# Kernel optimization log

Hardware: AMD Instinct MI355X
Metric: run time of the kernel (lower is better)

## Reference

```python
import jax, jax.numpy as jnp
import numpy as np

N = 100000   # nodes
E = 1000000  # directed edges (before self-loops)
G = 512      # graphs in the batch
NEG_SLOPE = 0.2
EPS = 1e-5


def setup_inputs() -> dict:
    key = jax.random.key(0)
    ks = jax.random.split(key, 24)
    r = lambda i, shape, s=0.1: (jax.random.normal(ks[i], shape) * s).astype(jnp.float32)
    return {
        'x': jax.random.normal(ks[0], (N, 27), dtype=jnp.float32),
        'edge_index': jax.random.randint(ks[1], (2, E), 0, N, dtype=jnp.int32),
        'batch': jnp.sort(jax.random.randint(ks[2], (N,), 0, G, dtype=jnp.int32)),
        # GATv2Conv(26, 32, heads=2)
        'Wl1': r(3, (26, 64)), 'bl1': jnp.zeros(64, jnp.float32),
        'Wr1': r(4, (26, 64)), 'br1': jnp.zeros(64, jnp.float32),
        'att1': r(5, (2, 32)), 'b1': jnp.zeros(64, jnp.float32),
        'g1': jnp.ones(64, jnp.float32), 'be1': jnp.zeros(64, jnp.float32),
        # GATv2Conv(64, 32, heads=1)
        'Wl2': r(6, (64, 32)), 'bl2': jnp.zeros(32, jnp.float32),
        'Wr2': r(7, (64, 32)), 'br2': jnp.zeros(32, jnp.float32),
        'att2': r(8, (1, 32)), 'b2': jnp.zeros(32, jnp.float32),
        'g2': jnp.ones(32, jnp.float32), 'be2': jnp.zeros(32, jnp.float32),
        # gate_nn: 32 -> 16 -> 1
        'Wg1': r(9, (32, 16)), 'bg1': jnp.zeros(16, jnp.float32),
        'Wg2': r(10, (16, 1)), 'bg2': jnp.zeros(1, jnp.float32),
        # final head: 33 -> 16 -> 1
        'Wh1': r(11, (33, 16)), 'bh1': jnp.zeros(16, jnp.float32),
        'Wh2': r(12, (16, 1)), 'bh2': jnp.zeros(1, jnp.float32),
    }


def _gatv2(x, Wl, bl, Wr, br, att, bias, src, dst, heads, ch):
    n = x.shape[0]
    xl = (x @ Wl + bl).reshape(n, heads, ch)  # source projection (messages)
    xr = (x @ Wr + br).reshape(n, heads, ch)  # target projection
    e = jax.nn.leaky_relu(xl[src] + xr[dst], NEG_SLOPE)      # [Etot, H, C]
    logits = jnp.einsum('ehc,hc->eh', e, att)                 # [Etot, H]
    m = jax.ops.segment_max(logits, dst, num_segments=n)
    a = jnp.exp(logits - m[dst])
    z = jax.ops.segment_sum(a, dst, num_segments=n)
    a = a / (z[dst] + 1e-16)
    out = jax.ops.segment_sum(xl[src] * a[:, :, None], dst, num_segments=n)
    return out.reshape(n, heads * ch) + bias


def _batchnorm(h, gamma, beta):
    mu = h.mean(axis=0)
    var = jnp.var(h, axis=0)  # biased, matches torch normalization
    return (h - mu) * jax.lax.rsqrt(var + EPS) * gamma + beta


def reference(x, edge_index, batch, Wl1, bl1, Wr1, br1, att1, b1, g1, be1,
              Wl2, bl2, Wr2, br2, att2, b2, g2, be2,
              Wg1, bg1, Wg2, bg2, Wh1, bh1, Wh2, bh2):
    n = x.shape[0]
    loops = jnp.arange(n, dtype=edge_index.dtype)
    src = jnp.concatenate([edge_index[0], loops])
    dst = jnp.concatenate([edge_index[1], loops])
    x_no_cost = jnp.concatenate([x[:, :24], x[:, 25:]], axis=1)  # [N, 26]
    h = jax.nn.elu(_batchnorm(_gatv2(x_no_cost, Wl1, bl1, Wr1, br1, att1, b1, src, dst, 2, 32), g1, be1))
    # dropout is identity in eval mode
    h = jax.nn.elu(_batchnorm(_gatv2(h, Wl2, bl2, Wr2, br2, att2, b2, src, dst, 1, 32), g2, be2))
    # attentional aggregation: gate MLP + segment softmax over graphs
    gate = jax.nn.relu(h @ Wg1 + bg1) @ Wg2 + bg2               # [N, 1]
    gm = jax.ops.segment_max(gate, batch, num_segments=G)
    ga = jnp.exp(gate - gm[batch])
    gz = jax.ops.segment_sum(ga, batch, num_segments=G)
    ga = ga / (gz[batch] + 1e-16)
    h_pooled = jax.ops.segment_sum(ga * h, batch, num_segments=G)  # [G, 32]
    counts = jax.ops.segment_sum(jnp.ones((n, 1), x.dtype), batch, num_segments=G)
    root_costs = jax.ops.segment_sum(x[:, 24:25], batch, num_segments=G) / jnp.maximum(counts, 1.0)
    combined = jnp.concatenate([h_pooled, root_costs], axis=1)   # [G, 33]
    return jax.nn.relu(combined @ Wh1 + bh1) @ Wh2 + bh2         # [G, 1]
```

## Files before the change

kernel.cpp:

```cpp
#include <hip/hip_runtime.h>
#include <hip/hip_fp16.h>
#include <math.h>

#define NEG 0.2f
#define BN_EPS 1e-5f
#define BKT_W 256
#define CHUNK 4096


__global__ __launch_bounds__(256, 4)
void hist_proj1_kernel(const int* __restrict__ ei, int E, int nbh, int nbkt,
                       int* __restrict__ cnt,
                       const float* __restrict__ in, int in_stride,
                       const float* __restrict__ Wl, const float* __restrict__ bl,
                       const float* __restrict__ Wr, const float* __restrict__ br,
                       __half* __restrict__ outl, __half* __restrict__ outr, int n)
{
    __shared__ int hist[512];
    __shared__ float xs[32][28];

    if (blockIdx.x < nbh) {
        const int bid = blockIdx.x;
        for (int i = threadIdx.x; i < nbkt; i += 256) hist[i] = 0;
        __syncthreads();
        const int g0 = bid * (CHUNK / 4);
        #pragma unroll
        for (int it = 0; it < CHUNK / 1024; ++it) {
            int e = (g0 + it * 256 + threadIdx.x) * 4;
            if (e + 3 < E) {
                int4 d4 = *(const int4*)(ei + E + e);
                atomicAdd(&hist[d4.x >> 8], 1);
                atomicAdd(&hist[d4.y >> 8], 1);
                atomicAdd(&hist[d4.z >> 8], 1);
                atomicAdd(&hist[d4.w >> 8], 1);
            } else {
                for (int k = 0; k < 4; ++k)
                    if (e + k < E) atomicAdd(&hist[ei[E + e + k] >> 8], 1);
            }
        }
        __syncthreads();
        for (int i = threadIdx.x; i < nbkt; i += 256) cnt[(size_t)i * nbh + bid] = hist[i];
    } else {
        constexpr int K = 26, OC = 64, NCG = 32;
        const int row0 = (blockIdx.x - nbh) * 32;
        for (int i = threadIdx.x; i < 32 * K; i += 256) {
            int r = i / K, k = i - r * K;
            int row = row0 + r;
            float v = 0.f;
            if (row < n) {
                int sc = (k < 24) ? k : k + 1;
                v = in[(size_t)row * in_stride + sc];
            }
            xs[r][k] = v;
        }
        __syncthreads();

        const int cg = threadIdx.x % NCG;
        const int rg = threadIdx.x / NCG;
        const int c4 = cg * 4;
        const bool left = (c4 < OC);
        const float* __restrict__ Wp = left ? Wl : Wr;
        const int cc = left ? c4 : c4 - OC;
        const float4 b4 = *(const float4*)((left ? bl : br) + cc);

        float acc[4][4];
        #pragma unroll
        for (int ri = 0; ri < 4; ++ri) {
            acc[ri][0] = b4.x; acc[ri][1] = b4.y; acc[ri][2] = b4.z; acc[ri][3] = b4.w;
        }
        #pragma unroll 1
        for (int kb = 0; kb < K / 4; ++kb) {
            const float4 w0 = *(const float4*)(Wp + (size_t)(kb * 4 + 0) * OC + cc);
            const float4 w1 = *(const float4*)(Wp + (size_t)(kb * 4 + 1) * OC + cc);
            const float4 w2 = *(const float4*)(Wp + (size_t)(kb * 4 + 2) * OC + cc);
            const float4 w3 = *(const float4*)(Wp + (size_t)(kb * 4 + 3) * OC + cc);
            #pragma unroll
            for (int ri = 0; ri < 4; ++ri) {
                const float4 xv = *(const float4*)(&xs[rg * 4 + ri][kb * 4]);
                acc[ri][0] += xv.x * w0.x + xv.y * w1.x + xv.z * w2.x + xv.w * w3.x;
                acc[ri][1] += xv.x * w0.y + xv.y * w1.y + xv.z * w2.y + xv.w * w3.y;
                acc[ri][2] += xv.x * w0.z + xv.y * w1.z + xv.z * w2.z + xv.w * w3.z;
                acc[ri][3] += xv.x * w0.w + xv.y * w1.w + xv.z * w2.w + xv.w * w3.w;
            }
        }
        #pragma unroll
        for (int k = 24; k < K; ++k) {
            const float4 wk = *(const float4*)(Wp + (size_t)k * OC + cc);
            #pragma unroll
            for (int ri = 0; ri < 4; ++ri) {
                const float xk = xs[rg * 4 + ri][k];
                acc[ri][0] += xk * wk.x; acc[ri][1] += xk * wk.y;
                acc[ri][2] += xk * wk.z; acc[ri][3] += xk * wk.w;
            }
        }
        __half* __restrict__ outp = left ? outl : outr;
        #pragma unroll
        for (int ri = 0; ri < 4; ++ri) {
            const int row = row0 + rg * 4 + ri;
            if (row >= n) continue;
            union { uint2 u; __half2 h[2]; } o;
            o.h[0] = __float22half2_rn(make_float2(acc[ri][0], acc[ri][1]));
            o.h[1] = __float22half2_rn(make_float2(acc[ri][2], acc[ri][3]));
            *(uint2*)(outp + (size_t)row * OC + cc) = o.u;
        }
    }
}

__global__ __launch_bounds__(256)
void scan_block_kernel(const int* __restrict__ in, int* __restrict__ out,
                       int* __restrict__ bsum, int n)
{
    __shared__ int s[256];
    int i = blockIdx.x * 256 + threadIdx.x;
    int v = (i < n) ? in[i] : 0;
    s[threadIdx.x] = v;
    __syncthreads();
    for (int off = 1; off < 256; off <<= 1) {
        int t = (threadIdx.x >= off) ? s[threadIdx.x - off] : 0;
        __syncthreads();
        s[threadIdx.x] += t;
        __syncthreads();
    }
    if (i < n) out[i + 1] = s[threadIdx.x];
    if (threadIdx.x == 255) bsum[blockIdx.x] = s[255];
}

__global__ __launch_bounds__(512)
void scan_sums_kernel(int* __restrict__ bsum, int nb)
{
    __shared__ int s[512];
    int v = (threadIdx.x < nb) ? bsum[threadIdx.x] : 0;
    s[threadIdx.x] = v;
    __syncthreads();
    for (int off = 1; off < 512; off <<= 1) {
        int t = (threadIdx.x >= off) ? s[threadIdx.x - off] : 0;
        __syncthreads();
        s[threadIdx.x] += t;
        __syncthreads();
    }
    if (threadIdx.x < nb) bsum[threadIdx.x] = s[threadIdx.x] - v;
}

__global__ __launch_bounds__(256)
void scan_add_kernel(int* __restrict__ out, const int* __restrict__ bsum, int n)
{
    int i = blockIdx.x * 256 + threadIdx.x;
    if (i < n) out[i + 1] += bsum[blockIdx.x];
    if (i == 0) out[0] = 0;
}

__global__ __launch_bounds__(256)
void scat_kernel(const int* __restrict__ ei, int E, int nbh, int nbkt,
                 const int* __restrict__ base, int2* __restrict__ pairs)
{
    __shared__ int fill[512];
    __shared__ int lbase[512];
    for (int i = threadIdx.x; i < nbkt; i += 256) {
        fill[i]  = 0;
        lbase[i] = base[(size_t)i * nbh + blockIdx.x];
    }
    __syncthreads();
    const int g0 = blockIdx.x * (CHUNK / 4);
    #pragma unroll
    for (int it = 0; it < CHUNK / 1024; ++it) {
        int e = (g0 + it * 256 + threadIdx.x) * 4;
        if (e + 3 < E) {
            int4 s4 = *(const int4*)(ei + e);
            int4 d4 = *(const int4*)(ei + E + e);
            int b, r;
            b = d4.x >> 8; r = atomicAdd(&fill[b], 1); pairs[lbase[b] + r] = make_int2(s4.x, d4.x);
            b = d4.y >> 8; r = atomicAdd(&fill[b], 1); pairs[lbase[b] + r] = make_int2(s4.y, d4.y);
            b = d4.z >> 8; r = atomicAdd(&fill[b], 1); pairs[lbase[b] + r] = make_int2(s4.z, d4.z);
            b = d4.w >> 8; r = atomicAdd(&fill[b], 1); pairs[lbase[b] + r] = make_int2(s4.w, d4.w);
        } else {
            for (int k = 0; k < 4; ++k) {
                if (e + k < E) {
                    int s = ei[e + k], d = ei[E + e + k];
                    int b = d >> 8;
                    int r = atomicAdd(&fill[b], 1);
                    pairs[lbase[b] + r] = make_int2(s, d);
                }
            }
        }
    }
}

__global__ __launch_bounds__(256)
void bucket_build_kernel(const int2* __restrict__ pairs, const int* __restrict__ base,
                         int nbh, int nbkt, int n, int E,
                         int* __restrict__ rowptr, int* __restrict__ srcs,
                         int* __restrict__ perm)
{
    const int b     = blockIdx.x;
    const int start = base[(size_t)b * nbh];
    const int end   = base[(size_t)(b + 1) * nbh];
    __shared__ int hist[256], sc[256], dcnt[64], dbase[64];
    hist[threadIdx.x] = 0;
    if (threadIdx.x < 64) dcnt[threadIdx.x] = 0;
    __syncthreads();
    for (int j = start + threadIdx.x; j < end; j += 256)
        atomicAdd(&hist[pairs[j].y & 255], 1);
    __syncthreads();
    const int v = hist[threadIdx.x];
    sc[threadIdx.x] = v;
    __syncthreads();
    for (int off = 1; off < 256; off <<= 1) {
        int t = (threadIdx.x >= off) ? sc[threadIdx.x - off] : 0;
        __syncthreads();
        sc[threadIdx.x] += t;
        __syncthreads();
    }
    const int excl = sc[threadIdx.x] - v;
    const int d = b * 256 + threadIdx.x;
    int bin = 0, rnk = 0;
    if (d < n) {
        rowptr[d] = start + excl;
        bin = min(v, 63);
        rnk = atomicAdd(&dcnt[bin], 1);
    }
    if (b == nbkt - 1 && threadIdx.x == 0) rowptr[n] = E;
    __syncthreads();
    hist[threadIdx.x] = excl;
    __syncthreads();
    for (int j = start + threadIdx.x; j < end; j += 256) {
        int2 p = pairs[j];
        int r = atomicAdd(&hist[p.y & 255], 1);
        srcs[start + r] = p.x;
    }
    if (threadIdx.x < 64) dbase[threadIdx.x] = dcnt[threadIdx.x];
    __syncthreads();
    for (int off = 1; off < 64; off <<= 1) {
        int t = 0;
        if (threadIdx.x < 64 && threadIdx.x >= off) t = dbase[threadIdx.x - off];
        __syncthreads();
        if (threadIdx.x < 64) dbase[threadIdx.x] += t;
        __syncthreads();
    }
    if (d < n) perm[b * 256 + (dbase[bin] - dcnt[bin]) + rnk] = d;
}


__device__ __forceinline__ void gat_step4(const uint2 raw, const float* __restrict__ xrv,
                                          const float* __restrict__ at,
                                          float& z, float* __restrict__ acc)
{
    union { uint2 u; __half2 h[2]; } q; q.u = raw;
    const float2 a = __half22float2(q.h[0]);
    const float2 b = __half22float2(q.h[1]);
    float t, p = 0.f;
    t = a.x + xrv[0]; t = t > 0.f ? t : NEG * t; p += t * at[0];
    t = a.y + xrv[1]; t = t > 0.f ? t : NEG * t; p += t * at[1];
    t = b.x + xrv[2]; t = t > 0.f ? t : NEG * t; p += t * at[2];
    t = b.y + xrv[3]; t = t > 0.f ? t : NEG * t; p += t * at[3];
    p += __shfl_xor(p, 1, 64);
    p += __shfl_xor(p, 2, 64);
    p += __shfl_xor(p, 4, 64);
    const float w = __expf(p);
    z += w;
    acc[0] += w * a.x; acc[1] += w * a.y; acc[2] += w * b.x; acc[3] += w * b.y;
}

template<int HC, bool OUT_HALF>
__global__ __launch_bounds__(256)
void gat_fused_kernel(const __half* __restrict__ xl, const __half* __restrict__ xr,
                      const float* __restrict__ att,
                      const int* __restrict__ rowptr, const int* __restrict__ srcs,
                      const int* __restrict__ perm,
                      void* __restrict__ outp, int n)
{
    constexpr int LPG = HC / 4;
    const int gid  = (blockIdx.x * 256 + threadIdx.x) / LPG;
    const int lane = threadIdx.x % LPG;
    if (gid >= n) return;
    const int d = perm[gid];

    float at[4], xrv[4];
    {
        const float4 a = *(const float4*)(att + lane * 4);
        at[0] = a.x; at[1] = a.y; at[2] = a.z; at[3] = a.w;
        union { uint2 u; __half2 h[2]; } qx;
        qx.u = *(const uint2*)(xr + (size_t)d * HC + lane * 4);
        const float2 x0 = __half22float2(qx.h[0]);
        const float2 x1 = __half22float2(qx.h[1]);
        xrv[0] = x0.x; xrv[1] = x0.y; xrv[2] = x1.x; xrv[3] = x1.y;
    }

    float z = 0.f, acc[4] = {0.f, 0.f, 0.f, 0.f};
    gat_step4(*(const uint2*)(xl + (size_t)d * HC + lane * 4), xrv, at, z, acc);

    const int jb = rowptr[d], je = rowptr[d + 1];
    int j = jb;
    for (; j + 4 <= je; j += 4) {
        const int s0 = srcs[j], s1 = srcs[j + 1], s2 = srcs[j + 2], s3 = srcs[j + 3];
        const uint2 r0 = *(const uint2*)(xl + (size_t)s0 * HC + lane * 4);
        const uint2 r1 = *(const uint2*)(xl + (size_t)s1 * HC + lane * 4);
        const uint2 r2 = *(const uint2*)(xl + (size_t)s2 * HC + lane * 4);
        const uint2 r3 = *(const uint2*)(xl + (size_t)s3 * HC + lane * 4);
        gat_step4(r0, xrv, at, z, acc);
        gat_step4(r1, xrv, at, z, acc);
        gat_step4(r2, xrv, at, z, acc);
        gat_step4(r3, xrv, at, z, acc);
    }
    for (; j < je; ++j)
        gat_step4(*(const uint2*)(xl + (size_t)srcs[j] * HC + lane * 4), xrv, at, z, acc);

    const float inv = 1.f / (z + 1e-16f);
    if constexpr (OUT_HALF) {
        union { uint2 u; __half2 h[2]; } o;
        o.h[0] = __float22half2_rn(make_float2(acc[0] * inv, acc[1] * inv));
        o.h[1] = __float22half2_rn(make_float2(acc[2] * inv, acc[3] * inv));
        *(uint2*)((__half*)outp + (size_t)d * HC + lane * 4) = o.u;
    } else {
        *(float4*)((float*)outp + (size_t)d * HC + lane * 4) =
            make_float4(acc[0] * inv, acc[1] * inv, acc[2] * inv, acc[3] * inv);
    }
}

template<int K, int OC>
__global__ __launch_bounds__(256, 4)
void proj2_kernel(const __half* __restrict__ in,
                  const float* __restrict__ Wl, const float* __restrict__ bl,
                  const float* __restrict__ Wr, const float* __restrict__ br,
                  const float* __restrict__ stats, const float* __restrict__ gamma,
                  const float* __restrict__ beta, float inv_n,
                  __half* __restrict__ outl, __half* __restrict__ outr, int n)
{
    constexpr int C2  = 2 * OC;
    constexpr int NCG = C2 / 4;
    constexpr int NRG = 256 / NCG;
    constexpr int TR  = NRG * 4;
    __shared__ float xs[TR][K];

    const int kk  = threadIdx.x % K;
    const float mu  = stats[kk] * inv_n;
    const float var = stats[K + kk] * inv_n - mu * mu;
    const float rs  = rsqrtf(var + BN_EPS) * gamma[kk];
    const float na = rs, nb = beta[kk] - mu * rs;

    const int row0 = blockIdx.x * TR;
    for (int i = threadIdx.x; i < TR * K; i += 256) {
        int r = i / K, k = i - r * K;
        int row = row0 + r;
        float v = 0.f;
        if (row < n) {
            float t = __half2float(in[(size_t)row * K + k]) * na + nb;
            v = t > 0.f ? t : expm1f(t);
        }
        xs[r][k] = v;
    }
    __syncthreads();

    const int cg = threadIdx.x % NCG;
    const int rg = threadIdx.x / NCG;
    const int c4 = cg * 4;
    const bool left = (c4 < OC);
    const float* __restrict__ Wp = left ? Wl : Wr;
    const int cc = left ? c4 : c4 - OC;
    const float4 b4 = *(const float4*)((left ? bl : br) + cc);

    float acc[4][4];
    #pragma unroll
    for (int ri = 0; ri < 4; ++ri) {
        acc[ri][0] = b4.x; acc[ri][1] = b4.y; acc[ri][2] = b4.z; acc[ri][3] = b4.w;
    }

    #pragma unroll 1
    for (int kb = 0; kb < K / 4; ++kb) {
        const float4 w0 = *(const float4*)(Wp + (size_t)(kb * 4 + 0) * OC + cc);
        const float4 w1 = *(const float4*)(Wp + (size_t)(kb * 4 + 1) * OC + cc);
        const float4 w2 = *(const float4*)(Wp + (size_t)(kb * 4 + 2) * OC + cc);
        const float4 w3 = *(const float4*)(Wp + (size_t)(kb * 4 + 3) * OC + cc);
        #pragma unroll
        for (int ri = 0; ri < 4; ++ri) {
            const float4 xv = *(const float4*)(&xs[rg * 4 + ri][kb * 4]);
            acc[ri][0] += xv.x * w0.x + xv.y * w1.x + xv.z * w2.x + xv.w * w3.x;
            acc[ri][1] += xv.x * w0.y + xv.y * w1.y + xv.z * w2.y + xv.w * w3.y;
            acc[ri][2] += xv.x * w0.z + xv.y * w1.z + xv.z * w2.z + xv.w * w3.z;
            acc[ri][3] += xv.x * w0.w + xv.y * w1.w + xv.z * w2.w + xv.w * w3.w;
        }
    }

    __half* __restrict__ outp = left ? outl : outr;
    #pragma unroll
    for (int ri = 0; ri < 4; ++ri) {
        const int row = row0 + rg * 4 + ri;
        if (row >= n) continue;
        union { uint2 u; __half2 h[2]; } o;
        o.h[0] = __float22half2_rn(make_float2(acc[ri][0], acc[ri][1]));
        o.h[1] = __float22half2_rn(make_float2(acc[ri][2], acc[ri][3]));
        *(uint2*)(outp + (size_t)row * OC + cc) = o.u;
    }
}

template<int C, bool IN_HALF>
__global__ __launch_bounds__(256)
void bn_stats_kernel(const void* __restrict__ h, int n, float* __restrict__ stats)
{
    constexpr int RPB = 256 / C;
    int col = threadIdx.x % C, rg = threadIdx.x / C;
    float s = 0.f, s2 = 0.f;
    for (int r = blockIdx.x * RPB + rg; r < n; r += gridDim.x * RPB) {
        float v;
        if constexpr (IN_HALF) v = __half2float(((const __half*)h)[(size_t)r * C + col]);
        else                   v = ((const float*)h)[(size_t)r * C + col];
        s += v; s2 += v * v;
    }
    __shared__ float red0[256], red1[256];
    red0[threadIdx.x] = s; red1[threadIdx.x] = s2;
    __syncthreads();
    for (int st = 128; st >= C; st >>= 1) {
        if (threadIdx.x < st) {
            red0[threadIdx.x] += red0[threadIdx.x + st];
            red1[threadIdx.x] += red1[threadIdx.x + st];
        }
        __syncthreads();
    }
    if (threadIdx.x < C) {
        atomicAdd(&stats[threadIdx.x],     red0[threadIdx.x]);
        atomicAdd(&stats[C + threadIdx.x], red1[threadIdx.x]);
    }
}

__global__ __launch_bounds__(256)
void gate_norm_kernel(float* __restrict__ h2, int n,
                      const float* __restrict__ stats, const float* __restrict__ gamma,
                      const float* __restrict__ beta, float inv_n,
                      const float* __restrict__ Wg1, const float* __restrict__ bg1,
                      const float* __restrict__ Wg2, const float* __restrict__ bg2,
                      float* __restrict__ gate)
{
    __shared__ float W1[512], W2[16], B1[16], A_[32], B_[32];
    for (int i = threadIdx.x; i < 512; i += 256) W1[i] = Wg1[i];
    if (threadIdx.x < 16) { W2[threadIdx.x] = Wg2[threadIdx.x]; B1[threadIdx.x] = bg1[threadIdx.x]; }
    if (threadIdx.x < 32) {
        float mu  = stats[threadIdx.x] * inv_n;
        float var = stats[32 + threadIdx.x] * inv_n - mu * mu;
        float rs  = rsqrtf(var + BN_EPS) * gamma[threadIdx.x];
        A_[threadIdx.x] = rs;
        B_[threadIdx.x] = beta[threadIdx.x] - mu * rs;
    }
    __syncthreads();
    int node = blockIdx.x * 256 + threadIdx.x;
    if (node >= n) return;
    float* row = h2 + (size_t)node * 32;
    float v[32];
    #pragma unroll
    for (int j = 0; j < 8; ++j) {
        float4 r = *(const float4*)(row + j * 4);
        v[4*j] = r.x; v[4*j+1] = r.y; v[4*j+2] = r.z; v[4*j+3] = r.w;
    }
    #pragma unroll
    for (int k = 0; k < 32; ++k) {
        float t = v[k] * A_[k] + B_[k];
        v[k] = t > 0.f ? t : expm1f(t);
    }
    float hid[16];
    #pragma unroll
    for (int j = 0; j < 16; ++j) hid[j] = B1[j];
    #pragma unroll
    for (int k = 0; k < 32; ++k) {
        #pragma unroll
        for (int j = 0; j < 16; ++j) hid[j] += v[k] * W1[k * 16 + j];
    }
    float g = bg2[0];
    #pragma unroll
    for (int j = 0; j < 16; ++j) g += (hid[j] > 0.f ? hid[j] : 0.f) * W2[j];
    gate[node] = g;
    #pragma unroll
    for (int j = 0; j < 8; ++j)
        *(float4*)(row + j * 4) = make_float4(v[4*j], v[4*j+1], v[4*j+2], v[4*j+3]);
}

__global__ __launch_bounds__(256)
void pool_head_kernel(const float* __restrict__ h2, const float* __restrict__ gate,
                      const int* __restrict__ batch, const float* __restrict__ x,
                      int n, int xstride,
                      const float* __restrict__ Wh1, const float* __restrict__ bh1,
                      const float* __restrict__ Wh2, const float* __restrict__ bh2,
                      float* __restrict__ out)
{
    int g = blockIdx.x;
    __shared__ int sstart, send;
    if (threadIdx.x == 0) {
        int lo = 0, hi = n;
        while (lo < hi) { int mid = (lo + hi) >> 1; if (batch[mid] < g) lo = mid + 1; else hi = mid; }
        sstart = lo;
        hi = n;
        while (lo < hi) { int mid = (lo + hi) >> 1; if (batch[mid] < g + 1) lo = mid + 1; else hi = mid; }
        send = lo;
    }
    __syncthreads();
    const int start = sstart, end = send, cnt = end - start;

    __shared__ float red[256];
    float mx = -INFINITY;
    for (int i = start + threadIdx.x; i < end; i += 256) mx = fmaxf(mx, gate[i]);
    red[threadIdx.x] = mx; __syncthreads();
    for (int st = 128; st > 0; st >>= 1) {
        if (threadIdx.x < st) red[threadIdx.x] = fmaxf(red[threadIdx.x], red[threadIdx.x + st]);
        __syncthreads();
    }
    const float gm = red[0]; __syncthreads();

    float se = 0.f;
    for (int i = start + threadIdx.x; i < end; i += 256) se += expf(gate[i] - gm);
    red[threadIdx.x] = se; __syncthreads();
    for (int st = 128; st > 0; st >>= 1) {
        if (threadIdx.x < st) red[threadIdx.x] += red[threadIdx.x + st];
        __syncthreads();
    }
    const float gz = red[0]; __syncthreads();

    float rc = 0.f;
    for (int i = start + threadIdx.x; i < end; i += 256) rc += x[(size_t)i * xstride + 24];
    red[threadIdx.x] = rc; __syncthreads();
    for (int st = 128; st > 0; st >>= 1) {
        if (threadIdx.x < st) red[threadIdx.x] += red[threadIdx.x + st];
        __syncthreads();
    }
    const float root = red[0] / fmaxf((float)cnt, 1.f); __syncthreads();

    const int col = threadIdx.x % 32, rg = threadIdx.x / 32;
    float acc = 0.f;
    for (int i = start + rg; i < end; i += 8) acc += expf(gate[i] - gm) * h2[(size_t)i * 32 + col];
    red[threadIdx.x] = acc; __syncthreads();
    for (int st = 128; st >= 32; st >>= 1) {
        if (threadIdx.x < st) red[threadIdx.x] += red[threadIdx.x + st];
        __syncthreads();
    }
    __shared__ float comb[33];
    if (threadIdx.x < 32) comb[threadIdx.x] = red[threadIdx.x] / (gz + 1e-16f);
    if (threadIdx.x == 0) comb[32] = root;
    __syncthreads();

    __shared__ float hidr[16];
    if (threadIdx.x < 16) {
        float hv = bh1[threadIdx.x];
        #pragma unroll
        for (int k = 0; k < 33; ++k) hv += comb[k] * Wh1[k * 16 + threadIdx.x];
        hidr[threadIdx.x] = hv > 0.f ? hv : 0.f;
    }
    __syncthreads();
    if (threadIdx.x == 0) {
        float r = bh2[0];
        #pragma unroll
        for (int j = 0; j < 16; ++j) r += hidr[j] * Wh2[j];
        out[g] = r;
    }
}


extern "C" void kernel_launch(void* const* d_in, const int* in_sizes, int n_in,
                              void* d_out, int out_size, void* d_ws, size_t ws_size,
                              hipStream_t stream)
{
    const float* x    = (const float*)d_in[0];
    const int*   ei   = (const int*)d_in[1];
    const int*   batch= (const int*)d_in[2];
    const float* Wl1  = (const float*)d_in[3];
    const float* bl1  = (const float*)d_in[4];
    const float* Wr1  = (const float*)d_in[5];
    const float* br1  = (const float*)d_in[6];
    const float* att1 = (const float*)d_in[7];
    const float* g1   = (const float*)d_in[9];
    const float* be1  = (const float*)d_in[10];
    const float* Wl2  = (const float*)d_in[11];
    const float* bl2  = (const float*)d_in[12];
    const float* Wr2  = (const float*)d_in[13];
    const float* br2  = (const float*)d_in[14];
    const float* att2 = (const float*)d_in[15];
    const float* g2   = (const float*)d_in[17];
    const float* be2  = (const float*)d_in[18];
    const float* Wg1  = (const float*)d_in[19];
    const float* bg1  = (const float*)d_in[20];
    const float* Wg2  = (const float*)d_in[21];
    const float* bg2  = (const float*)d_in[22];
    const float* Wh1  = (const float*)d_in[23];
    const float* bh1  = (const float*)d_in[24];
    const float* Wh2  = (const float*)d_in[25];
    const float* bh2  = (const float*)d_in[26];

    const int n  = in_sizes[0] / 27;
    const int E  = in_sizes[1] / 2;
    const int G  = out_size;
    const float inv_n = 1.f / (float)n;

    const int nbkt = (n + BKT_W - 1) / BKT_W;
    const int nbh  = (E + CHUNK - 1) / CHUNK;
    const int SZ   = nbkt * nbh;
    const int NBs  = (SZ + 255) / 256;
    const int npr1 = (n + 31) / 32;

    float* ws = (float*)d_ws;
    size_t off = 0;
    auto align4 = [&](size_t v) { return (v + 3) & ~(size_t)3; };
    float* st1 = ws + off; off += 128;
    float* st2 = ws + off; off += 64;
    const size_t zero_floats = off;
    int* cnt     = (int*)(ws + off); off = align4(off + SZ);
    int* basearr = (int*)(ws + off); off = align4(off + SZ + 1);
    int* bsum    = (int*)(ws + off); off = align4(off + 512);
    int* rowptr  = (int*)(ws + off); off = align4(off + n + 1);
    int* srcs    = (int*)(ws + off); off = align4(off + E);
    int* perm    = (int*)(ws + off); off = align4(off + n);
    __half* xl1h = (__half*)(ws + off); off += (size_t)n * 32;
    __half* xr1h = (__half*)(ws + off); off += (size_t)n * 32;
    __half* h1h  = (__half*)(ws + off); off += (size_t)n * 32;
    float* h2    = ws + off; off += (size_t)n * 32;
    float* gate  = ws + off; off += (size_t)n;
    int2* pairs   = (int2*)h1h;
    __half* xl2h  = xl1h;
    __half* xr2h  = xr1h;

    hipMemsetAsync(d_ws, 0, zero_floats * sizeof(float), stream);

    hist_proj1_kernel<<<nbh + npr1, 256, 0, stream>>>(
        ei, E, nbh, nbkt, cnt, x, 27, Wl1, bl1, Wr1, br1, xl1h, xr1h, n);
    scan_block_kernel<<<NBs, 256, 0, stream>>>(cnt, basearr, bsum, SZ);
    scan_sums_kernel<<<1, 512, 0, stream>>>(bsum, NBs);
    scan_add_kernel<<<NBs, 256, 0, stream>>>(basearr, bsum, SZ);
    scat_kernel<<<nbh, 256, 0, stream>>>(ei, E, nbh, nbkt, basearr, pairs);
    bucket_build_kernel<<<nbkt, 256, 0, stream>>>(pairs, basearr, nbh, nbkt, n, E, rowptr, srcs, perm);

    gat_fused_kernel<64, true><<<(n * 16 + 255) / 256, 256, 0, stream>>>(
        xl1h, xr1h, att1, rowptr, srcs, perm, h1h, n);
    bn_stats_kernel<64, true><<<1024, 256, 0, stream>>>(h1h, n, st1);

    proj2_kernel<64, 32><<<(n + 63) / 64, 256, 0, stream>>>(
        h1h, Wl2, bl2, Wr2, br2, st1, g1, be1, inv_n, xl2h, xr2h, n);
    gat_fused_kernel<32, false><<<(n * 8 + 255) / 256, 256, 0, stream>>>(
        xl2h, xr2h, att2, rowptr, srcs, perm, h2, n);
    bn_stats_kernel<32, false><<<1024, 256, 0, stream>>>(h2, n, st2);

    gate_norm_kernel<<<(n + 255) / 256, 256, 0, stream>>>(
        h2, n, st2, g2, be2, inv_n, Wg1, bg1, Wg2, bg2, gate);
    pool_head_kernel<<<G, 256, 0, stream>>>(h2, gate, batch, x, n, 27, Wh1, bh1, Wh2, bh2, (float*)d_out);
}
```

Measured before the change: 264.6 us.

## Pack edge pairs into 32-bit ints, drop scan-add pass, split hist/proj1

Scattered edge pairs are packed into a single int (source shifted left with the low destination byte), halving the traffic written in the scatter pass and read in the bucket build. The separate scan-add kernel is removed; consumers compute exclusive bucket bases on the fly from the block-local scan and the block sums. The combined histogram/projection kernel is split into a standalone histogram kernel and a projection kernel launched after the CSR build. Packing limits node indices to 24 bits.

Result: no change. 266.3 us (+0.6%).

```diff
diff --git a/kernel.cpp b/kernel.cpp
--- a/kernel.cpp
+++ b/kernel.cpp
@@ -8,102 +8,29 @@
 #define CHUNK 4096
 
 
-__global__ __launch_bounds__(256, 4)
-void hist_proj1_kernel(const int* __restrict__ ei, int E, int nbh, int nbkt,
-                       int* __restrict__ cnt,
-                       const float* __restrict__ in, int in_stride,
-                       const float* __restrict__ Wl, const float* __restrict__ bl,
-                       const float* __restrict__ Wr, const float* __restrict__ br,
-                       __half* __restrict__ outl, __half* __restrict__ outr, int n)
+__global__ __launch_bounds__(256)
+void hist_kernel(const int* __restrict__ ei, int E, int nbh, int nbkt, int* __restrict__ cnt)
 {
     __shared__ int hist[512];
-    __shared__ float xs[32][28];
-
-    if (blockIdx.x < nbh) {
-        const int bid = blockIdx.x;
-        for (int i = threadIdx.x; i < nbkt; i += 256) hist[i] = 0;
-        __syncthreads();
-        const int g0 = bid * (CHUNK / 4);
-        #pragma unroll
-        for (int it = 0; it < CHUNK / 1024; ++it) {
-            int e = (g0 + it * 256 + threadIdx.x) * 4;
-            if (e + 3 < E) {
-                int4 d4 = *(const int4*)(ei + E + e);
-                atomicAdd(&hist[d4.x >> 8], 1);
-                atomicAdd(&hist[d4.y >> 8], 1);
-                atomicAdd(&hist[d4.z >> 8], 1);
-                atomicAdd(&hist[d4.w >> 8], 1);
-            } else {
-                for (int k = 0; k < 4; ++k)
-                    if (e + k < E) atomicAdd(&hist[ei[E + e + k] >> 8], 1);
-            }
-        }
-        __syncthreads();
-        for (int i = threadIdx.x; i < nbkt; i += 256) cnt[(size_t)i * nbh + bid] = hist[i];
-    } else {
-        constexpr int K = 26, OC = 64, NCG = 32;
-        const int row0 = (blockIdx.x - nbh) * 32;
-        for (int i = threadIdx.x; i < 32 * K; i += 256) {
-            int r = i / K, k = i - r * K;
-            int row = row0 + r;
-            float v = 0.f;
-            if (row < n) {
-                int sc = (k < 24) ? k : k + 1;
-                v = in[(size_t)row * in_stride + sc];
-            }
-            xs[r][k] = v;
-        }
-        __syncthreads();
-
-        const int cg = threadIdx.x % NCG;
-        const int rg = threadIdx.x / NCG;
-        const int c4 = cg * 4;
-        const bool left = (c4 < OC);
-        const float* __restrict__ Wp = left ? Wl : Wr;
-        const int cc = left ? c4 : c4 - OC;
-        const float4 b4 = *(const float4*)((left ? bl : br) + cc);
-
-        float acc[4][4];
-        #pragma unroll
-        for (int ri = 0; ri < 4; ++ri) {
-            acc[ri][0] = b4.x; acc[ri][1] = b4.y; acc[ri][2] = b4.z; acc[ri][3] = b4.w;
-        }
-        #pragma unroll 1
-        for (int kb = 0; kb < K / 4; ++kb) {
-            const float4 w0 = *(const float4*)(Wp + (size_t)(kb * 4 + 0) * OC + cc);
-            const float4 w1 = *(const float4*)(Wp + (size_t)(kb * 4 + 1) * OC + cc);
-            const float4 w2 = *(const float4*)(Wp + (size_t)(kb * 4 + 2) * OC + cc);
-            const float4 w3 = *(const float4*)(Wp + (size_t)(kb * 4 + 3) * OC + cc);
-            #pragma unroll
-            for (int ri = 0; ri < 4; ++ri) {
-                const float4 xv = *(const float4*)(&xs[rg * 4 + ri][kb * 4]);
-                acc[ri][0] += xv.x * w0.x + xv.y * w1.x + xv.z * w2.x + xv.w * w3.x;
-                acc[ri][1] += xv.x * w0.y + xv.y * w1.y + xv.z * w2.y + xv.w * w3.y;
-                acc[ri][2] += xv.x * w0.z + xv.y * w1.z + xv.z * w2.z + xv.w * w3.z;
-                acc[ri][3] += xv.x * w0.w + xv.y * w1.w + xv.z * w2.w + xv.w * w3.w;
-            }
-        }
-        #pragma unroll
-        for (int k = 24; k < K; ++k) {
-            const float4 wk = *(const float4*)(Wp + (size_t)k * OC + cc);
-            #pragma unroll
-            for (int ri = 0; ri < 4; ++ri) {
-                const float xk = xs[rg * 4 + ri][k];
-                acc[ri][0] += xk * wk.x; acc[ri][1] += xk * wk.y;
-                acc[ri][2] += xk * wk.z; acc[ri][3] += xk * wk.w;
-            }
-        }
-        __half* __restrict__ outp = left ? outl : outr;
-        #pragma unroll
-        for (int ri = 0; ri < 4; ++ri) {
-            const int row = row0 + rg * 4 + ri;
-            if (row >= n) continue;
-            union { uint2 u; __half2 h[2]; } o;
-            o.h[0] = __float22half2_rn(make_float2(acc[ri][0], acc[ri][1]));
-            o.h[1] = __float22half2_rn(make_float2(acc[ri][2], acc[ri][3]));
-            *(uint2*)(outp + (size_t)row * OC + cc) = o.u;
-        }
-    }
+    for (int i = threadIdx.x; i < nbkt; i += 256) hist[i] = 0;
+    __syncthreads();
+    const int g0 = blockIdx.x * (CHUNK / 4);
+    #pragma unroll
+    for (int it = 0; it < CHUNK / 1024; ++it) {
+        int e = (g0 + it * 256 + threadIdx.x) * 4;
+        if (e + 3 < E) {
+            int4 d4 = *(const int4*)(ei + E + e);
+            atomicAdd(&hist[d4.x >> 8], 1);
+            atomicAdd(&hist[d4.y >> 8], 1);
+            atomicAdd(&hist[d4.z >> 8], 1);
+            atomicAdd(&hist[d4.w >> 8], 1);
+        } else {
+            for (int k = 0; k < 4; ++k)
+                if (e + k < E) atomicAdd(&hist[ei[E + e + k] >> 8], 1);
+        }
+    }
+    __syncthreads();
+    for (int i = threadIdx.x; i < nbkt; i += 256) cnt[(size_t)i * nbh + blockIdx.x] = hist[i];
 }
 
 __global__ __launch_bounds__(256)
@@ -141,23 +68,22 @@
     if (threadIdx.x < nb) bsum[threadIdx.x] = s[threadIdx.x] - v;
 }
 
-__global__ __launch_bounds__(256)
-void scan_add_kernel(int* __restrict__ out, const int* __restrict__ bsum, int n)
-{
-    int i = blockIdx.x * 256 + threadIdx.x;
-    if (i < n) out[i + 1] += bsum[blockIdx.x];
-    if (i == 0) out[0] = 0;
+__device__ __forceinline__ int csr_base(const int* __restrict__ raw,
+                                        const int* __restrict__ bsum, int j)
+{
+    return (j == 0) ? 0 : raw[j] + bsum[(j - 1) >> 8];
 }
 
 __global__ __launch_bounds__(256)
 void scat_kernel(const int* __restrict__ ei, int E, int nbh, int nbkt,
-                 const int* __restrict__ base, int2* __restrict__ pairs)
+                 const int* __restrict__ raw, const int* __restrict__ bsum,
+                 int* __restrict__ pairs)
 {
     __shared__ int fill[512];
     __shared__ int lbase[512];
     for (int i = threadIdx.x; i < nbkt; i += 256) {
         fill[i]  = 0;
-        lbase[i] = base[(size_t)i * nbh + blockIdx.x];
+        lbase[i] = csr_base(raw, bsum, i * nbh + blockIdx.x);
     }
     __syncthreads();
     const int g0 = blockIdx.x * (CHUNK / 4);
@@ -168,17 +94,17 @@
             int4 s4 = *(const int4*)(ei + e);
             int4 d4 = *(const int4*)(ei + E + e);
             int b, r;
-            b = d4.x >> 8; r = atomicAdd(&fill[b], 1); pairs[lbase[b] + r] = make_int2(s4.x, d4.x);
-            b = d4.y >> 8; r = atomicAdd(&fill[b], 1); pairs[lbase[b] + r] = make_int2(s4.y, d4.y);
-            b = d4.z >> 8; r = atomicAdd(&fill[b], 1); pairs[lbase[b] + r] = make_int2(s4.z, d4.z);
-            b = d4.w >> 8; r = atomicAdd(&fill[b], 1); pairs[lbase[b] + r] = make_int2(s4.w, d4.w);
+            b = d4.x >> 8; r = atomicAdd(&fill[b], 1); pairs[lbase[b] + r] = (s4.x << 8) | (d4.x & 255);
+            b = d4.y >> 8; r = atomicAdd(&fill[b], 1); pairs[lbase[b] + r] = (s4.y << 8) | (d4.y & 255);
+            b = d4.z >> 8; r = atomicAdd(&fill[b], 1); pairs[lbase[b] + r] = (s4.z << 8) | (d4.z & 255);
+            b = d4.w >> 8; r = atomicAdd(&fill[b], 1); pairs[lbase[b] + r] = (s4.w << 8) | (d4.w & 255);
         } else {
             for (int k = 0; k < 4; ++k) {
                 if (e + k < E) {
                     int s = ei[e + k], d = ei[E + e + k];
                     int b = d >> 8;
                     int r = atomicAdd(&fill[b], 1);
-                    pairs[lbase[b] + r] = make_int2(s, d);
+                    pairs[lbase[b] + r] = (s << 8) | (d & 255);
                 }
             }
         }
@@ -186,20 +112,21 @@
 }
 
 __global__ __launch_bounds__(256)
-void bucket_build_kernel(const int2* __restrict__ pairs, const int* __restrict__ base,
+void bucket_build_kernel(const int* __restrict__ pairs, const int* __restrict__ raw,
+                         const int* __restrict__ bsum,
                          int nbh, int nbkt, int n, int E,
                          int* __restrict__ rowptr, int* __restrict__ srcs,
                          int* __restrict__ perm)
 {
     const int b     = blockIdx.x;
-    const int start = base[(size_t)b * nbh];
-    const int end   = base[(size_t)(b + 1) * nbh];
+    const int start = csr_base(raw, bsum, b * nbh);
+    const int end   = csr_base(raw, bsum, (b + 1) * nbh);
     __shared__ int hist[256], sc[256], dcnt[64], dbase[64];
     hist[threadIdx.x] = 0;
     if (threadIdx.x < 64) dcnt[threadIdx.x] = 0;
     __syncthreads();
     for (int j = start + threadIdx.x; j < end; j += 256)
-        atomicAdd(&hist[pairs[j].y & 255], 1);
+        atomicAdd(&hist[pairs[j] & 255], 1);
     __syncthreads();
     const int v = hist[threadIdx.x];
     sc[threadIdx.x] = v;
@@ -223,9 +150,9 @@
     hist[threadIdx.x] = excl;
     __syncthreads();
     for (int j = start + threadIdx.x; j < end; j += 256) {
-        int2 p = pairs[j];
-        int r = atomicAdd(&hist[p.y & 255], 1);
-        srcs[start + r] = p.x;
+        int p = pairs[j];
+        int r = atomicAdd(&hist[p & 255], 1);
+        srcs[start + r] = ((unsigned)p) >> 8;
     }
     if (threadIdx.x < 64) dbase[threadIdx.x] = dcnt[threadIdx.x];
     __syncthreads();
@@ -313,6 +240,77 @@
     } else {
         *(float4*)((float*)outp + (size_t)d * HC + lane * 4) =
             make_float4(acc[0] * inv, acc[1] * inv, acc[2] * inv, acc[3] * inv);
+    }
+}
+
+__global__ __launch_bounds__(256, 4)
+void proj1_kernel(const float* __restrict__ in, int in_stride,
+                  const float* __restrict__ Wl, const float* __restrict__ bl,
+                  const float* __restrict__ Wr, const float* __restrict__ br,
+                  __half* __restrict__ outl, __half* __restrict__ outr, int n)
+{
+    constexpr int K = 26, OC = 64, NCG = 32;
+    __shared__ float xs[32][28];
+    const int row0 = blockIdx.x * 32;
+    for (int i = threadIdx.x; i < 32 * K; i += 256) {
+        int r = i / K, k = i - r * K;
+        int row = row0 + r;
+        float v = 0.f;
+        if (row < n) {
+            int sc = (k < 24) ? k : k + 1;
+            v = in[(size_t)row * in_stride + sc];
+        }
+        xs[r][k] = v;
+    }
+    __syncthreads();
+
+    const int cg = threadIdx.x % NCG;
+    const int rg = threadIdx.x / NCG;
+    const int c4 = cg * 4;
+    const bool left = (c4 < OC);
+    const float* __restrict__ Wp = left ? Wl : Wr;
+    const int cc = left ? c4 : c4 - OC;
+    const float4 b4 = *(const float4*)((left ? bl : br) + cc);
+
+    float acc[4][4];
+    #pragma unroll
+    for (int ri = 0; ri < 4; ++ri) {
+        acc[ri][0] = b4.x; acc[ri][1] = b4.y; acc[ri][2] = b4.z; acc[ri][3] = b4.w;
+    }
+    #pragma unroll 1
+    for (int kb = 0; kb < K / 4; ++kb) {
+        const float4 w0 = *(const float4*)(Wp + (size_t)(kb * 4 + 0) * OC + cc);
+        const float4 w1 = *(const float4*)(Wp + (size_t)(kb * 4 + 1) * OC + cc);
+        const float4 w2 = *(const float4*)(Wp + (size_t)(kb * 4 + 2) * OC + cc);
+        const float4 w3 = *(const float4*)(Wp + (size_t)(kb * 4 + 3) * OC + cc);
+        #pragma unroll
+        for (int ri = 0; ri < 4; ++ri) {
+            const float4 xv = *(const float4*)(&xs[rg * 4 + ri][kb * 4]);
+            acc[ri][0] += xv.x * w0.x + xv.y * w1.x + xv.z * w2.x + xv.w * w3.x;
+            acc[ri][1] += xv.x * w0.y + xv.y * w1.y + xv.z * w2.y + xv.w * w3.y;
+            acc[ri][2] += xv.x * w0.z + xv.y * w1.z + xv.z * w2.z + xv.w * w3.z;
+            acc[ri][3] += xv.x * w0.w + xv.y * w1.w + xv.z * w2.w + xv.w * w3.w;
+        }
+    }
+    #pragma unroll
+    for (int k = 24; k < K; ++k) {
+        const float4 wk = *(const float4*)(Wp + (size_t)k * OC + cc);
+        #pragma unroll
+        for (int ri = 0; ri < 4; ++ri) {
+            const float xk = xs[rg * 4 + ri][k];
+            acc[ri][0] += xk * wk.x; acc[ri][1] += xk * wk.y;
+            acc[ri][2] += xk * wk.z; acc[ri][3] += xk * wk.w;
+        }
+    }
+    __half* __restrict__ outp = left ? outl : outr;
+    #pragma unroll
+    for (int ri = 0; ri < 4; ++ri) {
+        const int row = row0 + rg * 4 + ri;
+        if (row >= n) continue;
+        union { uint2 u; __half2 h[2]; } o;
+        o.h[0] = __float22half2_rn(make_float2(acc[ri][0], acc[ri][1]));
+        o.h[1] = __float22half2_rn(make_float2(acc[ri][2], acc[ri][3]));
+        *(uint2*)(outp + (size_t)row * OC + cc) = o.u;
     }
 }
 
@@ -589,7 +587,6 @@
     const int nbh  = (E + CHUNK - 1) / CHUNK;
     const int SZ   = nbkt * nbh;
     const int NBs  = (SZ + 255) / 256;
-    const int npr1 = (n + 31) / 32;
 
     float* ws = (float*)d_ws;
     size_t off = 0;
@@ -608,20 +605,20 @@
     __half* h1h  = (__half*)(ws + off); off += (size_t)n * 32;
     float* h2    = ws + off; off += (size_t)n * 32;
     float* gate  = ws + off; off += (size_t)n;
-    int2* pairs   = (int2*)h1h;
+    int* pairs    = (int*)h1h;
     __half* xl2h  = xl1h;
     __half* xr2h  = xr1h;
 
     hipMemsetAsync(d_ws, 0, zero_floats * sizeof(float), stream);
 
-    hist_proj1_kernel<<<nbh + npr1, 256, 0, stream>>>(
-        ei, E, nbh, nbkt, cnt, x, 27, Wl1, bl1, Wr1, br1, xl1h, xr1h, n);
+    hist_kernel<<<nbh, 256, 0, stream>>>(ei, E, nbh, nbkt, cnt);
     scan_block_kernel<<<NBs, 256, 0, stream>>>(cnt, basearr, bsum, SZ);
     scan_sums_kernel<<<1, 512, 0, stream>>>(bsum, NBs);
-    scan_add_kernel<<<NBs, 256, 0, stream>>>(basearr, bsum, SZ);
-    scat_kernel<<<nbh, 256, 0, stream>>>(ei, E, nbh, nbkt, basearr, pairs);
-    bucket_build_kernel<<<nbkt, 256, 0, stream>>>(pairs, basearr, nbh, nbkt, n, E, rowptr, srcs, perm);
-
+    scat_kernel<<<nbh, 256, 0, stream>>>(ei, E, nbh, nbkt, basearr, bsum, pairs);
+    bucket_build_kernel<<<nbkt, 256, 0, stream>>>(pairs, basearr, bsum, nbh, nbkt, n, E, rowptr, srcs, perm);
+
+    proj1_kernel<<<(n + 31) / 32, 256, 0, stream>>>(
+        x, 27, Wl1, bl1, Wr1, br1, xl1h, xr1h, n);
     gat_fused_kernel<64, true><<<(n * 16 + 255) / 256, 256, 0, stream>>>(
         xl1h, xr1h, att1, rowptr, srcs, perm, h1h, n);
     bn_stats_kernel<64, true><<<1024, 256, 0, stream>>>(h1h, n, st1);
```
